# Optimization experiments

Measured on AMD Instinct MI355X. Metric: run time of the kernel, lower is better.

Reference implementation:

```python
import jax, jax.numpy as jnp
import numpy as np

NF = 10      # num RBF / Chebyshev features
GAMMA = 1.0
EMB = 10
H = 64
NHEADS = 2


def _rbf(d):
    centers = jnp.arange(1, NF + 1, dtype=d.dtype)
    return jnp.exp(-GAMMA * (centers - d[..., None]) ** 2)


def _cheb(a):
    feats = [jnp.ones_like(a), a]
    for _ in range(2, NF):
        feats.append(2 * a * feats[-1] - feats[-2])
    return jnp.stack(feats, -1)


def _gru_layer(xs, wih, whh, bih, bhh):
    # xs: [L, B, D] -> [L, B, H]; PyTorch gate order r, z, n
    B = xs.shape[1]
    def step(h, xt):
        gi = xt @ wih.T + bih
        gh = h @ whh.T + bhh
        ir, iz, inn = jnp.split(gi, 3, -1)
        hr, hz, hn = jnp.split(gh, 3, -1)
        r = jax.nn.sigmoid(ir + hr)
        z = jax.nn.sigmoid(iz + hz)
        n = jnp.tanh(inn + r * hn)
        hnew = (1 - z) * n + z * h
        return hnew, hnew
    h0 = jnp.zeros((B, H), xs.dtype)
    _, ys = jax.lax.scan(step, h0, xs)
    return ys


def _mha(x, in_w, in_b, out_w, out_b):
    B, L, E = x.shape
    hd = E // NHEADS
    qkv = x @ in_w.T + in_b
    q, k, v = jnp.split(qkv, 3, -1)
    sp = lambda t: t.reshape(B, L, NHEADS, hd).transpose(0, 2, 1, 3)
    q, k, v = sp(q), sp(k), sp(v)
    scale = 1.0 / float(np.sqrt(hd))
    att = jax.nn.softmax(jnp.einsum('bhqd,bhkd->bhqk', q, k) * scale, -1)
    o = jnp.einsum('bhqk,bhkd->bhqd', att, v).transpose(0, 2, 1, 3).reshape(B, L, E)
    return o @ out_w.T + out_b


def _ln(x, s, b):
    m = x.mean(-1, keepdims=True)
    v = ((x - m) ** 2).mean(-1, keepdims=True)
    return (x - m) / jnp.sqrt(v + 1e-5) * s + b


def setup_inputs() -> dict:
    key = jax.random.key(0)
    ks = jax.random.split(key, 48)
    N, L = 384, 256
    # bond rows: [atom_idx1, atom_idx2, bond_dist]; angle rows: [d1, d2, angle]
    idx1 = jax.random.randint(ks[0], (N, L), 1, 119).astype(jnp.float32)
    idx2 = jax.random.randint(ks[1], (N, L), 1, 119).astype(jnp.float32)
    dist = jax.random.uniform(ks[2], (N, L), minval=0.5, maxval=5.0)
    d1 = jax.random.uniform(ks[3], (N, L), minval=0.5, maxval=5.0)
    d2 = jax.random.uniform(ks[4], (N, L), minval=0.5, maxval=5.0)
    ang = jax.random.uniform(ks[5], (N, L), minval=-1.0, maxval=1.0)
    bond_x = jnp.stack([idx1, idx2, dist], 1)
    angle_x = jnp.stack([d1, d2, ang], 1)
    is_angle = (jnp.arange(N) % 3 == 2)
    x = jnp.where(is_angle[:, None, None], angle_x, bond_x)

    def nrm(k, shp, s=0.1):
        return jax.random.normal(k, shp) * s

    D_IN = 2 * EMB + NF  # 30
    inp = {
        'x': x,
        'emb': nrm(ks[6], (119, EMB), 1.0),
        'wih0': nrm(ks[7], (3 * H, D_IN)),
        'whh0': nrm(ks[8], (3 * H, H)),
        'bih0': nrm(ks[9], (3 * H,)),
        'bhh0': nrm(ks[10], (3 * H,)),
        'wih12': nrm(ks[11], (2, 3 * H, H)),
        'whh12': nrm(ks[12], (2, 3 * H, H)),
        'bih12': nrm(ks[13], (2, 3 * H)),
        'bhh12': nrm(ks[14], (2, 3 * H)),
        'in_w1': nrm(ks[15], (3 * H, H)),
        'in_b1': nrm(ks[16], (3 * H,)),
        'out_w1': nrm(ks[17], (H, H)),
        'out_b1': nrm(ks[18], (H,)),
        'in_w2': nrm(ks[19], (3 * H, H)),
        'in_b2': nrm(ks[20], (3 * H,)),
        'out_w2': nrm(ks[21], (H, H)),
        'out_b2': nrm(ks[22], (H,)),
        'ff_w1': nrm(ks[23], (1024, H)),
        'ff_b1': nrm(ks[24], (1024,)),
        'ff_w2': nrm(ks[25], (H, 1024)),
        'ff_b2': nrm(ks[26], (H,)),
        'ln1_s': jnp.ones((H,)), 'ln1_b': jnp.zeros((H,)),
        'ln2_s': jnp.ones((H,)), 'ln2_b': jnp.zeros((H,)),
        'ln3_s': jnp.ones((H,)), 'ln3_b': jnp.zeros((H,)),
        'ln4_s': jnp.ones((H,)), 'ln4_b': jnp.zeros((H,)),
        'fw1': nrm(ks[27], (256, H)), 'fb1': nrm(ks[28], (256,)),
        'fw2': nrm(ks[29], (64, 256)), 'fb2': nrm(ks[30], (64,)),
        'fw3': nrm(ks[31], (32, 64)), 'fb3': nrm(ks[32], (32,)),
        'fw4': nrm(ks[33], (1, 32)), 'fb4': nrm(ks[34], (1,)),
    }
    return inp


def reference(x, emb, wih0, whh0, bih0, bhh0, wih12, whh12, bih12, bhh12,
              in_w1, in_b1, out_w1, out_b1, in_w2, in_b2, out_w2, out_b2,
              ff_w1, ff_b1, ff_w2, ff_b2,
              ln1_s, ln1_b, ln2_s, ln2_b, ln3_s, ln3_b, ln4_s, ln4_b,
              fw1, fb1, fw2, fb2, fw3, fb3, fw4, fb4):
    # Vectorized featurization (replaces the per-triplet Python loop):
    # rows with i%3 in {0,1} are bond rows, i%3==2 are angle rows.
    i1 = jnp.clip(x[:, 0].astype(jnp.int32), 0, 118)
    i2 = jnp.clip(x[:, 1].astype(jnp.int32), 0, 118)
    bond_feat = jnp.concatenate([emb[i1], emb[i2], _rbf(x[:, 2])], -1)
    angle_feat = jnp.concatenate([_rbf(x[:, 0]), _rbf(x[:, 1]), _cheb(x[:, 2])], -1)
    is_angle = (jnp.arange(x.shape[0]) % 3 == 2)
    feat = jnp.where(is_angle[:, None, None], angle_feat, bond_feat)  # [N, L, 30]

    hs = feat.transpose(1, 0, 2)  # [L, N, 30]
    hs = _gru_layer(hs, wih0, whh0, bih0, bhh0)
    for l in range(2):
        hs = _gru_layer(hs, wih12[l], whh12[l], bih12[l], bhh12[l])
    g = hs.transpose(1, 0, 2)  # [N, L, H]

    def ffn(t):
        return jax.nn.relu(jax.nn.relu(t @ ff_w1.T + ff_b1) @ ff_w2.T + ff_b2)

    a = _mha(g, in_w1, in_b1, out_w1, out_b1)
    h = _ln(g + a, ln1_s, ln1_b)
    h = _ln(h + ffn(h), ln2_s, ln2_b)
    a = _mha(h, in_w2, in_b2, out_w2, out_b2)
    h = _ln(a + a, ln3_s, ln3_b)  # faithful to original: attn_out + attn_out
    h = _ln(h + ffn(h), ln4_s, ln4_b)
    o = h[:, -1, :]
    o = jax.nn.silu(o @ fw1.T + fb1)
    o = jax.nn.silu(o @ fw2.T + fb2)
    o = jax.nn.silu(o @ fw3.T + fb3)
    o = o @ fw4.T + fb4
    return o.squeeze(-1)
```

## Files before the change

kernel.cpp:

```cpp
#include <hip/hip_runtime.h>

static constexpr int NB   = 384;
static constexpr int SEQL = 256;
static constexpr int NROWS = NB * SEQL;

typedef short bf16x8 __attribute__((ext_vector_type(8)));
typedef float f32x4  __attribute__((ext_vector_type(4)));

union B8u {
    bf16x8 v;
    ushort us[8];
    uint4  q;
};

union F4u { float4 v; float f[4]; };

__device__ inline ushort f2bf(float f) {
    uint u = __float_as_uint(f);
    uint r = u + 0x7FFFu + ((u >> 16) & 1u);
    return (ushort)(r >> 16);
}

__device__ inline void split8(float4 a, float4 b, B8u& hi, B8u& lo) {
    float f[8] = {a.x, a.y, a.z, a.w, b.x, b.y, b.z, b.w};
    #pragma unroll
    for (int i = 0; i < 8; ++i) {
        ushort h = f2bf(f[i]);
        hi.us[i] = h;
        float fh = __uint_as_float(((uint)h) << 16);
        lo.us[i] = f2bf(f[i] - fh);
    }
}

__global__ __launch_bounds__(256) void split_kernel(
    const float* __restrict__ src, ushort* __restrict__ hi,
    ushort* __restrict__ lo, int n)
{
    int i = blockIdx.x * 256 + threadIdx.x;
    if (i < n) {
        float f = src[i];
        ushort h = f2bf(f);
        hi[i] = h;
        float fh = __uint_as_float(((uint)h) << 16);
        lo[i] = f2bf(f - fh);
    }
}

__global__ __launch_bounds__(192) void featproj_kernel(
    const float* __restrict__ x, const float* __restrict__ emb,
    const float* __restrict__ wih0, const float* __restrict__ bih0,
    float* __restrict__ X)
{
    __shared__ float F[32][33];
    const int tid = threadIdx.x;
    const int m0  = blockIdx.x * 32;

    if (tid < 96) {
        const int r   = tid & 31;
        const int grp = tid >> 5;
        const int m   = m0 + r;
        const int b   = m % NB;
        const int l   = m / NB;
        const float* xb = x + (size_t)b * (3 * SEQL);
        const float x0 = xb[l], x1 = xb[SEQL + l], x2 = xb[2 * SEQL + l];
        const bool is_angle = (b % 3) == 2;
        float o[10];
        if (is_angle) {
            if (grp < 2) {
                const float a = (grp == 0) ? x0 : x1;
                #pragma unroll
                for (int c = 0; c < 10; ++c) { float d = (float)(c + 1) - a; o[c] = __expf(-d * d); }
            } else {
                float t0 = 1.f, t1 = x2;
                o[0] = 1.f; o[1] = x2;
                #pragma unroll
                for (int c = 2; c < 10; ++c) { float t = 2.f * x2 * t1 - t0; o[c] = t; t0 = t1; t1 = t; }
            }
        } else {
            if (grp < 2) {
                const float xv = (grp == 0) ? x0 : x1;
                int idx = (int)xv; idx = idx < 0 ? 0 : (idx > 118 ? 118 : idx);
                #pragma unroll
                for (int c = 0; c < 10; ++c) o[c] = emb[idx * 10 + c];
            } else {
                #pragma unroll
                for (int c = 0; c < 10; ++c) { float d = (float)(c + 1) - x2; o[c] = __expf(-d * d); }
            }
        }
        #pragma unroll
        for (int c = 0; c < 10; ++c) F[r][grp * 10 + c] = o[c];
    }
    __syncthreads();

    float w[30];
    #pragma unroll
    for (int k = 0; k < 30; ++k) w[k] = wih0[tid * 30 + k];
    const float bj = bih0[tid];
    for (int r = 0; r < 32; ++r) {
        float acc = bj;
        #pragma unroll
        for (int k = 0; k < 30; ++k) acc += F[r][k] * w[k];
        X[(size_t)(m0 + r) * 192 + tid] = acc;
    }
}

__global__ __launch_bounds__(256, 1) void gru_mfma(
    const float* __restrict__ X, const ushort* __restrict__ WhhHi,
    const ushort* __restrict__ WhhLo, const float* __restrict__ bhh,
    float* __restrict__ Y, int out_batch_major)
{
    constexpr int PAD = 88;
    __shared__ __align__(16) ushort Hh[2][16][PAD];
    __shared__ __align__(16) ushort Hl[2][16][PAD];

    const int tid  = threadIdx.x;
    const int wt   = tid >> 6;
    const int lane = tid & 63;
    const int c    = lane & 15;
    const int g    = lane >> 4;
    const int b0   = blockIdx.x * 16;

    B8u awh[3][2], awl[3][2];
    #pragma unroll
    for (int gam = 0; gam < 3; ++gam)
        #pragma unroll
        for (int ks = 0; ks < 2; ++ks) {
            size_t off = (size_t)(64 * gam + 16 * wt + c) * 64 + 32 * ks + 8 * g;
            awh[gam][ks].q = *(const uint4*)(WhhHi + off);
            awl[gam][ks].q = *(const uint4*)(WhhLo + off);
        }
    float bg[3][4];
    #pragma unroll
    for (int gam = 0; gam < 3; ++gam)
        #pragma unroll
        for (int r = 0; r < 4; ++r)
            bg[gam][r] = bhh[64 * gam + 16 * wt + 4 * g + r];

    {
        ushort* zh = &Hh[0][0][0];
        ushort* zl = &Hl[0][0][0];
        for (int i = tid; i < 2 * 16 * PAD; i += 256) { zh[i] = 0; zl[i] = 0; }
    }
    float hold[4] = {0.f, 0.f, 0.f, 0.f};

    F4u gi[3];
    {
        const float* xp = X + ((size_t)(b0 + c)) * 192;
        #pragma unroll
        for (int gam = 0; gam < 3; ++gam)
            gi[gam].v = *(const float4*)(xp + 64 * gam + 16 * wt + 4 * g);
    }
    __syncthreads();

    for (int t = 0; t < SEQL; ++t) {
        const int p = t & 1;

        B8u bh[2], bl[2];
        #pragma unroll
        for (int ks = 0; ks < 2; ++ks) {
            const int sl = (4 * ks + g) ^ (c & 7);
            bh[ks].q = *(const uint4*)&Hh[p][c][sl * 8];
            bl[ks].q = *(const uint4*)&Hl[p][c][sl * 8];
        }

        f32x4 acc[3];
        #pragma unroll
        for (int gam = 0; gam < 3; ++gam)
            acc[gam] = (f32x4){bg[gam][0], bg[gam][1], bg[gam][2], bg[gam][3]};
        #pragma unroll
        for (int gam = 0; gam < 3; ++gam)
            #pragma unroll
            for (int ks = 0; ks < 2; ++ks) {
                acc[gam] = __builtin_amdgcn_mfma_f32_16x16x32_bf16(awh[gam][ks].v, bh[ks].v, acc[gam], 0, 0, 0);
                acc[gam] = __builtin_amdgcn_mfma_f32_16x16x32_bf16(awl[gam][ks].v, bh[ks].v, acc[gam], 0, 0, 0);
                acc[gam] = __builtin_amdgcn_mfma_f32_16x16x32_bf16(awh[gam][ks].v, bl[ks].v, acc[gam], 0, 0, 0);
            }

        F4u ngi[3];
        {
            const int tn = (t + 1 < SEQL) ? t + 1 : t;
            const float* xp = X + ((size_t)tn * NB + b0 + c) * 192;
            #pragma unroll
            for (int gam = 0; gam < 3; ++gam)
                ngi[gam].v = *(const float4*)(xp + 64 * gam + 16 * wt + 4 * g);
        }

        float hn4[4];
        #pragma unroll
        for (int r = 0; r < 4; ++r) {
            const float rr = 1.f / (1.f + __expf(-(gi[0].f[r] + acc[0][r])));
            const float zz = 1.f / (1.f + __expf(-(gi[1].f[r] + acc[1][r])));
            const float nn = tanhf(gi[2].f[r] + rr * acc[2][r]);
            hn4[r] = (1.f - zz) * nn + zz * hold[r];
            hold[r] = hn4[r];
        }

        {
            const size_t row = out_batch_major ? ((size_t)(b0 + c) * SEQL + t)
                                               : ((size_t)t * NB + b0 + c);
            *(float4*)&Y[row * 64 + 16 * wt + 4 * g] =
                make_float4(hn4[0], hn4[1], hn4[2], hn4[3]);
        }

        {
            ushort hh[4], hl[4];
            #pragma unroll
            for (int r = 0; r < 4; ++r) {
                ushort h = f2bf(hn4[r]);
                hh[r] = h;
                hl[r] = f2bf(hn4[r] - __uint_as_float(((uint)h) << 16));
            }
            const int sl = (2 * wt + (g >> 1)) ^ (c & 7);
            const int ad = sl * 8 + (g & 1) * 4;
            *(uint2*)&Hh[p ^ 1][c][ad] = make_uint2((uint)hh[0] | ((uint)hh[1] << 16),
                                                    (uint)hh[2] | ((uint)hh[3] << 16));
            *(uint2*)&Hl[p ^ 1][c][ad] = make_uint2((uint)hl[0] | ((uint)hl[1] << 16),
                                                    (uint)hl[2] | ((uint)hl[3] << 16));
        }
        #pragma unroll
        for (int gam = 0; gam < 3; ++gam) gi[gam].v = ngi[gam].v;
        __syncthreads();
    }
}

template<int NCOLS>
__global__ __launch_bounds__(256, 2) void gemm_mfma(
    const float* __restrict__ A, const ushort* __restrict__ Whi,
    const ushort* __restrict__ Wlo, const float* __restrict__ bias,
    float* __restrict__ C)
{
    const int tid = threadIdx.x;
    const int w   = tid >> 6;
    const int lane = tid & 63;
    const int c = lane & 15;
    const int g = lane >> 4;
    const int m0 = blockIdx.x * 128 + 32 * w;

    B8u ah[2][2], al[2][2];
    #pragma unroll
    for (int rm = 0; rm < 2; ++rm) {
        const float* ap = A + (size_t)(m0 + 16 * rm + c) * 64;
        #pragma unroll
        for (int ks = 0; ks < 2; ++ks) {
            float4 v0 = *(const float4*)(ap + 32 * ks + 8 * g);
            float4 v1 = *(const float4*)(ap + 32 * ks + 8 * g + 4);
            split8(v0, v1, ah[rm][ks], al[rm][ks]);
        }
    }

    f32x4 acc[NCOLS / 16][2];
    #pragma unroll
    for (int nt = 0; nt < NCOLS / 16; ++nt) {
        float bv = bias[16 * nt + c];
        #pragma unroll
        for (int rm = 0; rm < 2; ++rm)
            acc[nt][rm] = (f32x4){bv, bv, bv, bv};
    }

    #pragma unroll
    for (int nt = 0; nt < NCOLS / 16; ++nt) {
        B8u wh[2], wl[2];
        #pragma unroll
        for (int ks = 0; ks < 2; ++ks) {
            size_t off = (size_t)(16 * nt + c) * 64 + 32 * ks + 8 * g;
            wh[ks].q = *(const uint4*)(Whi + off);
            wl[ks].q = *(const uint4*)(Wlo + off);
        }
        #pragma unroll
        for (int rm = 0; rm < 2; ++rm)
            #pragma unroll
            for (int ks = 0; ks < 2; ++ks) {
                acc[nt][rm] = __builtin_amdgcn_mfma_f32_16x16x32_bf16(ah[rm][ks].v, wh[ks].v, acc[nt][rm], 0, 0, 0);
                acc[nt][rm] = __builtin_amdgcn_mfma_f32_16x16x32_bf16(al[rm][ks].v, wh[ks].v, acc[nt][rm], 0, 0, 0);
                acc[nt][rm] = __builtin_amdgcn_mfma_f32_16x16x32_bf16(ah[rm][ks].v, wl[ks].v, acc[nt][rm], 0, 0, 0);
            }
    }

    #pragma unroll
    for (int nt = 0; nt < NCOLS / 16; ++nt)
        #pragma unroll
        for (int rm = 0; rm < 2; ++rm)
            #pragma unroll
            for (int reg = 0; reg < 4; ++reg) {
                int row = m0 + 16 * rm + 4 * g + reg;
                C[(size_t)row * NCOLS + 16 * nt + c] = acc[nt][rm][reg];
            }
}

__global__ __launch_bounds__(256, 2) void ffn_mfma(
    const float* __restrict__ Xin,
    const ushort* __restrict__ W1hi, const ushort* __restrict__ W1lo,
    const ushort* __restrict__ W2hi, const ushort* __restrict__ W2lo,
    const float* __restrict__ b1, const float* __restrict__ b2,
    float* __restrict__ Out)
{
    __shared__ __align__(16) ushort sW1h[64 * 72], sW1l[64 * 72];
    __shared__ __align__(16) ushort sW2h[64 * 72], sW2l[64 * 72];
    __shared__ __align__(16) ushort sHh[128 * 72], sHl[128 * 72];
    __shared__ float sb1[64];

    const int tid = threadIdx.x;
    const int w   = tid >> 6;
    const int lane = tid & 63;
    const int c = lane & 15;
    const int g = lane >> 4;
    const int r0 = blockIdx.x * 128;

    B8u xh[2][2], xl[2][2];
    #pragma unroll
    for (int rm = 0; rm < 2; ++rm) {
        const float* ap = Xin + (size_t)(r0 + 32 * w + 16 * rm + c) * 64;
        #pragma unroll
        for (int ks = 0; ks < 2; ++ks) {
            float4 v0 = *(const float4*)(ap + 32 * ks + 8 * g);
            float4 v1 = *(const float4*)(ap + 32 * ks + 8 * g + 4);
            split8(v0, v1, xh[rm][ks], xl[rm][ks]);
        }
    }

    f32x4 acc2[4][2];
    #pragma unroll
    for (int jt = 0; jt < 4; ++jt) {
        float bv = b2[16 * jt + c];
        #pragma unroll
        for (int mt = 0; mt < 2; ++mt)
            acc2[jt][mt] = (f32x4){bv, bv, bv, bv};
    }

    for (int nc = 0; nc < 16; ++nc) {
        __syncthreads();
        {
            const int n = tid >> 2, s = tid & 3;
            size_t s1 = (size_t)(nc * 64 + n) * 64 + s * 16;
            size_t s2 = (size_t)n * 1024 + nc * 64 + s * 16;
            int d = n * 72 + s * 16;
            *(uint4*)&sW1h[d]     = *(const uint4*)(W1hi + s1);
            *(uint4*)&sW1h[d + 8] = *(const uint4*)(W1hi + s1 + 8);
            *(uint4*)&sW1l[d]     = *(const uint4*)(W1lo + s1);
            *(uint4*)&sW1l[d + 8] = *(const uint4*)(W1lo + s1 + 8);
            *(uint4*)&sW2h[d]     = *(const uint4*)(W2hi + s2);
            *(uint4*)&sW2h[d + 8] = *(const uint4*)(W2hi + s2 + 8);
            *(uint4*)&sW2l[d]     = *(const uint4*)(W2lo + s2);
            *(uint4*)&sW2l[d + 8] = *(const uint4*)(W2lo + s2 + 8);
            if (tid < 64) sb1[tid] = b1[nc * 64 + tid];
        }
        __syncthreads();

        f32x4 acc1[4][2];
        #pragma unroll
        for (int jm = 0; jm < 4; ++jm) {
            float b0 = sb1[16 * jm + 4 * g + 0];
            float b1v = sb1[16 * jm + 4 * g + 1];
            float b2v = sb1[16 * jm + 4 * g + 2];
            float b3v = sb1[16 * jm + 4 * g + 3];
            #pragma unroll
            for (int rm = 0; rm < 2; ++rm)
                acc1[jm][rm] = (f32x4){b0, b1v, b2v, b3v};
        }
        #pragma unroll
        for (int jm = 0; jm < 4; ++jm) {
            B8u w1h[2], w1l[2];
            #pragma unroll
            for (int ks = 0; ks < 2; ++ks) {
                int off = (16 * jm + c) * 72 + 32 * ks + 8 * g;
                w1h[ks].q = *(const uint4*)&sW1h[off];
                w1l[ks].q = *(const uint4*)&sW1l[off];
            }
            #pragma unroll
            for (int rm = 0; rm < 2; ++rm)
                #pragma unroll
                for (int ks = 0; ks < 2; ++ks) {
                    acc1[jm][rm] = __builtin_amdgcn_mfma_f32_16x16x32_bf16(w1h[ks].v, xh[rm][ks].v, acc1[jm][rm], 0, 0, 0);
                    acc1[jm][rm] = __builtin_amdgcn_mfma_f32_16x16x32_bf16(w1l[ks].v, xh[rm][ks].v, acc1[jm][rm], 0, 0, 0);
                    acc1[jm][rm] = __builtin_amdgcn_mfma_f32_16x16x32_bf16(w1h[ks].v, xl[rm][ks].v, acc1[jm][rm], 0, 0, 0);
                }
        }
        #pragma unroll
        for (int jm = 0; jm < 4; ++jm)
            #pragma unroll
            for (int rm = 0; rm < 2; ++rm) {
                ushort hh[4], hl[4];
                #pragma unroll
                for (int reg = 0; reg < 4; ++reg) {
                    float hv = fmaxf(acc1[jm][rm][reg], 0.f);
                    ushort h = f2bf(hv);
                    hh[reg] = h;
                    float fh = __uint_as_float(((uint)h) << 16);
                    hl[reg] = f2bf(hv - fh);
                }
                int el = (32 * w + 16 * rm + c) * 72 + 16 * jm + 4 * g;
                *(uint2*)&sHh[el] = make_uint2((uint)hh[0] | ((uint)hh[1] << 16),
                                               (uint)hh[2] | ((uint)hh[3] << 16));
                *(uint2*)&sHl[el] = make_uint2((uint)hl[0] | ((uint)hl[1] << 16),
                                               (uint)hl[2] | ((uint)hl[3] << 16));
            }
        asm volatile("s_waitcnt lgkmcnt(0)" ::: "memory");
        __builtin_amdgcn_sched_barrier(0);

        #pragma unroll
        for (int ks = 0; ks < 2; ++ks) {
            B8u ahh[2], ahl[2], bwh[4], bwl[4];
            #pragma unroll
            for (int mt = 0; mt < 2; ++mt) {
                int el = (32 * w + 16 * mt + c) * 72 + 32 * ks + 8 * g;
                ahh[mt].q = *(const uint4*)&sHh[el];
                ahl[mt].q = *(const uint4*)&sHl[el];
            }
            #pragma unroll
            for (int jt = 0; jt < 4; ++jt) {
                int el = (16 * jt + c) * 72 + 32 * ks + 8 * g;
                bwh[jt].q = *(const uint4*)&sW2h[el];
                bwl[jt].q = *(const uint4*)&sW2l[el];
            }
            #pragma unroll
            for (int jt = 0; jt < 4; ++jt)
                #pragma unroll
                for (int mt = 0; mt < 2; ++mt) {
                    acc2[jt][mt] = __builtin_amdgcn_mfma_f32_16x16x32_bf16(ahh[mt].v, bwh[jt].v, acc2[jt][mt], 0, 0, 0);
                    acc2[jt][mt] = __builtin_amdgcn_mfma_f32_16x16x32_bf16(ahl[mt].v, bwh[jt].v, acc2[jt][mt], 0, 0, 0);
                    acc2[jt][mt] = __builtin_amdgcn_mfma_f32_16x16x32_bf16(ahh[mt].v, bwl[jt].v, acc2[jt][mt], 0, 0, 0);
                }
        }
    }

    #pragma unroll
    for (int jt = 0; jt < 4; ++jt)
        #pragma unroll
        for (int mt = 0; mt < 2; ++mt)
            #pragma unroll
            for (int reg = 0; reg < 4; ++reg) {
                int row = r0 + 32 * w + 16 * mt + 4 * g + reg;
                Out[(size_t)row * 64 + 16 * jt + c] = fmaxf(acc2[jt][mt][reg], 0.f);
            }
}

__global__ __launch_bounds__(256, 2) void attn_mfma(
    const float* __restrict__ QKV, float* __restrict__ Out)
{
    __shared__ __align__(16) ushort Ph[4][4096];
    __shared__ __align__(16) ushort Pl[4][4096];

    const int h = blockIdx.x;
    const int b = blockIdx.y;
    const int tid = threadIdx.x;
    const int w = tid >> 6;
    const int lane = tid & 63;
    const int c = lane & 15;
    const int g = lane >> 4;
    const float scale = 0.17677669529663687f;

    const float* base = QKV + (size_t)b * SEQL * 192;
    ushort* phw = Ph[w];
    ushort* plw = Pl[w];

    B8u qh[4], ql[4];
    #pragma unroll
    for (int qt = 0; qt < 4; ++qt) {
        const float* p = base + (size_t)(64 * w + 16 * qt + c) * 192 + h * 32 + 8 * g;
        float4 v0 = *(const float4*)p;
        float4 v1 = *(const float4*)(p + 4);
        v0.x *= scale; v0.y *= scale; v0.z *= scale; v0.w *= scale;
        v1.x *= scale; v1.y *= scale; v1.z *= scale; v1.w *= scale;
        split8(v0, v1, qh[qt], ql[qt]);
    }

    f32x4 o[2][4];
    #pragma unroll
    for (int dt = 0; dt < 2; ++dt)
        #pragma unroll
        for (int qt = 0; qt < 4; ++qt)
            o[dt][qt] = (f32x4){0.f, 0.f, 0.f, 0.f};
    float mrun[4] = {-1e30f, -1e30f, -1e30f, -1e30f};
    float lrun[4] = {0.f, 0.f, 0.f, 0.f};

    for (int kc = 0; kc < 4; ++kc) {
        B8u kh[4], kl[4];
        #pragma unroll
        for (int kt = 0; kt < 4; ++kt) {
            const float* p = base + (size_t)(kc * 64 + 16 * kt + c) * 192 + 64 + h * 32 + 8 * g;
            split8(*(const float4*)p, *(const float4*)(p + 4), kh[kt], kl[kt]);
        }
        f32x4 st[4][4];
        #pragma unroll
        for (int kt = 0; kt < 4; ++kt)
            #pragma unroll
            for (int qt = 0; qt < 4; ++qt)
                st[kt][qt] = (f32x4){0.f, 0.f, 0.f, 0.f};
        #pragma unroll
        for (int kt = 0; kt < 4; ++kt)
            #pragma unroll
            for (int qt = 0; qt < 4; ++qt) {
                st[kt][qt] = __builtin_amdgcn_mfma_f32_16x16x32_bf16(kh[kt].v, qh[qt].v, st[kt][qt], 0, 0, 0);
                st[kt][qt] = __builtin_amdgcn_mfma_f32_16x16x32_bf16(kl[kt].v, qh[qt].v, st[kt][qt], 0, 0, 0);
                st[kt][qt] = __builtin_amdgcn_mfma_f32_16x16x32_bf16(kh[kt].v, ql[qt].v, st[kt][qt], 0, 0, 0);
            }

        asm volatile("s_waitcnt lgkmcnt(0)" ::: "memory");
        #pragma unroll
        for (int qt = 0; qt < 4; ++qt) {
            float cmax = st[0][qt][0];
            #pragma unroll
            for (int kt = 0; kt < 4; ++kt)
                #pragma unroll
                for (int r = 0; r < 4; ++r) cmax = fmaxf(cmax, st[kt][qt][r]);
            cmax = fmaxf(cmax, __shfl_xor(cmax, 16));
            cmax = fmaxf(cmax, __shfl_xor(cmax, 32));
            const float mnew = fmaxf(mrun[qt], cmax);
            const float corr = __expf(mrun[qt] - mnew);
            mrun[qt] = mnew;
            const int ql_ = 16 * qt + c;
            float csum = 0.f;
            #pragma unroll
            for (int kt = 0; kt < 4; ++kt) {
                ushort hh[4], hl[4];
                #pragma unroll
                for (int r = 0; r < 4; ++r) {
                    float pv = __expf(st[kt][qt][r] - mnew);
                    csum += pv;
                    ushort ph_ = f2bf(pv);
                    hh[r] = ph_;
                    hl[r] = f2bf(pv - __uint_as_float(((uint)ph_) << 16));
                }
                const int ow = (2 * kt + (g >> 1)) ^ (ql_ & 7);
                const int addr = ql_ * 64 + ow * 8 + (g & 1) * 4;
                *(uint2*)&phw[addr] = make_uint2((uint)hh[0] | ((uint)hh[1] << 16),
                                                 (uint)hh[2] | ((uint)hh[3] << 16));
                *(uint2*)&plw[addr] = make_uint2((uint)hl[0] | ((uint)hl[1] << 16),
                                                 (uint)hl[2] | ((uint)hl[3] << 16));
            }
            csum += __shfl_xor(csum, 16);
            csum += __shfl_xor(csum, 32);
            lrun[qt] = lrun[qt] * corr + csum;
            #pragma unroll
            for (int dt = 0; dt < 2; ++dt)
                #pragma unroll
                for (int r = 0; r < 4; ++r) o[dt][qt][r] *= corr;
        }

        B8u vh[2][2], vl[2][2];
        #pragma unroll
        for (int ks = 0; ks < 2; ++ks)
            #pragma unroll
            for (int dt = 0; dt < 2; ++dt) {
                const float* vp = base + (size_t)(kc * 64 + ks * 32 + 8 * g) * 192 + 128 + h * 32 + 16 * dt + c;
                float f0 = vp[0], f1 = vp[192], f2 = vp[384], f3 = vp[576];
                float f4 = vp[768], f5 = vp[960], f6 = vp[1152], f7 = vp[1344];
                split8(make_float4(f0, f1, f2, f3), make_float4(f4, f5, f6, f7),
                       vh[ks][dt], vl[ks][dt]);
            }

        asm volatile("s_waitcnt lgkmcnt(0)" ::: "memory");
        __builtin_amdgcn_sched_barrier(0);

        #pragma unroll
        for (int ks = 0; ks < 2; ++ks)
            #pragma unroll
            for (int qt = 0; qt < 4; ++qt) {
                const int ql_ = 16 * qt + c;
                const int orr = (ks * 4 + g) ^ (ql_ & 7);
                const int addr = ql_ * 64 + orr * 8;
                B8u pbh, pbl;
                pbh.q = *(const uint4*)&phw[addr];
                pbl.q = *(const uint4*)&plw[addr];
                #pragma unroll
                for (int dt = 0; dt < 2; ++dt) {
                    o[dt][qt] = __builtin_amdgcn_mfma_f32_16x16x32_bf16(vh[ks][dt].v, pbh.v, o[dt][qt], 0, 0, 0);
                    o[dt][qt] = __builtin_amdgcn_mfma_f32_16x16x32_bf16(vl[ks][dt].v, pbh.v, o[dt][qt], 0, 0, 0);
                    o[dt][qt] = __builtin_amdgcn_mfma_f32_16x16x32_bf16(vh[ks][dt].v, pbl.v, o[dt][qt], 0, 0, 0);
                }
            }
    }

    #pragma unroll
    for (int qt = 0; qt < 4; ++qt) {
        const float inv = 1.f / lrun[qt];
        const size_t row = (size_t)b * SEQL + 64 * w + 16 * qt + c;
        #pragma unroll
        for (int dt = 0; dt < 2; ++dt)
            #pragma unroll
            for (int r = 0; r < 4; ++r)
                Out[row * 64 + h * 32 + 16 * dt + 4 * g + r] = o[dt][qt][r] * inv;
    }
}

__global__ __launch_bounds__(256) void add_ln_kernel(
    const float* __restrict__ A, const float* __restrict__ B,
    const float* __restrict__ s, const float* __restrict__ bb,
    float* __restrict__ O)
{
    const size_t row = (size_t)blockIdx.x * 4 + (threadIdx.x >> 6);
    const int lane = threadIdx.x & 63;
    float v = A[row * 64 + lane] + B[row * 64 + lane];
    float sum = v;
    #pragma unroll
    for (int off = 32; off; off >>= 1) sum += __shfl_xor(sum, off);
    const float mean = sum * (1.f / 64.f);
    const float d = v - mean;
    float sq = d * d;
    #pragma unroll
    for (int off = 32; off; off >>= 1) sq += __shfl_xor(sq, off);
    const float var = sq * (1.f / 64.f);
    O[row * 64 + lane] = d * rsqrtf(var + 1e-5f) * s[lane] + bb[lane];
}

__global__ __launch_bounds__(256) void head_kernel(
    const float* __restrict__ Hf,
    const float* __restrict__ fw1, const float* __restrict__ fb1,
    const float* __restrict__ fw2, const float* __restrict__ fb2,
    const float* __restrict__ fw3, const float* __restrict__ fb3,
    const float* __restrict__ fw4, const float* __restrict__ fb4,
    float* __restrict__ out)
{
    const int b = blockIdx.x;
    const int tid = threadIdx.x;
    __shared__ float t0[64], t1[256], t2[64], t3[32];
    if (tid < 64) t0[tid] = Hf[((size_t)b * SEQL + (SEQL - 1)) * 64 + tid];
    __syncthreads();
    {
        float acc = fb1[tid];
        #pragma unroll 4
        for (int k = 0; k < 64; ++k) acc += t0[k] * fw1[tid * 64 + k];
        t1[tid] = acc / (1.f + __expf(-acc));
    }
    __syncthreads();
    if (tid < 64) {
        float acc = fb2[tid];
        #pragma unroll 4
        for (int k = 0; k < 256; ++k) acc += t1[k] * fw2[tid * 256 + k];
        t2[tid] = acc / (1.f + __expf(-acc));
    }
    __syncthreads();
    if (tid < 32) {
        float acc = fb3[tid];
        #pragma unroll 4
        for (int k = 0; k < 64; ++k) acc += t2[k] * fw3[tid * 64 + k];
        t3[tid] = acc / (1.f + __expf(-acc));
    }
    __syncthreads();
    if (tid == 0) {
        float acc = fb4[0];
        #pragma unroll
        for (int k = 0; k < 32; ++k) acc += t3[k] * fw4[k];
        out[b] = acc;
    }
}

extern "C" void kernel_launch(void* const* d_in, const int* in_sizes, int n_in,
                              void* d_out, int out_size, void* d_ws, size_t ws_size,
                              hipStream_t stream) {
    const float* x     = (const float*)d_in[0];
    const float* emb   = (const float*)d_in[1];
    const float* wih0  = (const float*)d_in[2];
    const float* whh0  = (const float*)d_in[3];
    const float* bih0  = (const float*)d_in[4];
    const float* bhh0  = (const float*)d_in[5];
    const float* wih12 = (const float*)d_in[6];
    const float* whh12 = (const float*)d_in[7];
    const float* bih12 = (const float*)d_in[8];
    const float* bhh12 = (const float*)d_in[9];
    const float* in_w1 = (const float*)d_in[10];
    const float* in_b1 = (const float*)d_in[11];
    const float* out_w1= (const float*)d_in[12];
    const float* out_b1= (const float*)d_in[13];
    const float* in_w2 = (const float*)d_in[14];
    const float* in_b2 = (const float*)d_in[15];
    const float* out_w2= (const float*)d_in[16];
    const float* out_b2= (const float*)d_in[17];
    const float* ff_w1 = (const float*)d_in[18];
    const float* ff_b1 = (const float*)d_in[19];
    const float* ff_w2 = (const float*)d_in[20];
    const float* ff_b2 = (const float*)d_in[21];
    const float* ln1_s = (const float*)d_in[22];
    const float* ln1_b = (const float*)d_in[23];
    const float* ln2_s = (const float*)d_in[24];
    const float* ln2_b = (const float*)d_in[25];
    const float* ln3_s = (const float*)d_in[26];
    const float* ln3_b = (const float*)d_in[27];
    const float* ln4_s = (const float*)d_in[28];
    const float* ln4_b = (const float*)d_in[29];
    const float* fw1   = (const float*)d_in[30];
    const float* fb1   = (const float*)d_in[31];
    const float* fw2   = (const float*)d_in[32];
    const float* fb2   = (const float*)d_in[33];
    const float* fw3   = (const float*)d_in[34];
    const float* fb3   = (const float*)d_in[35];
    const float* fw4   = (const float*)d_in[36];
    const float* fb4   = (const float*)d_in[37];

    float* ws = (float*)d_ws;
    float* X  = ws;
    float* S0 = X  + (size_t)NROWS * 192;
    float* S1 = S0 + (size_t)NROWS * 64;
    float* S2 = S1 + (size_t)NROWS * 64;

    ushort* bf = (ushort*)(S2 + (size_t)NROWS * 64);
    ushort* ffw1hi = bf;
    ushort* ffw1lo = ffw1hi + 65536;
    ushort* ffw2hi = ffw1lo + 65536;
    ushort* ffw2lo = ffw2hi + 65536;
    ushort* wghi   = ffw2lo + 65536;
    ushort* wglo   = wghi + 24576;
    ushort* q1hi   = wglo + 24576;
    ushort* q1lo   = q1hi + 12288;
    ushort* q2hi   = q1lo + 12288;
    ushort* q2lo   = q2hi + 12288;
    ushort* o1hi   = q2lo + 12288;
    ushort* o1lo   = o1hi + 4096;
    ushort* o2hi   = o1lo + 4096;
    ushort* o2lo   = o2hi + 4096;
    ushort* w0hi   = o2lo + 4096;
    ushort* w0lo   = w0hi + 12288;
    ushort* w12hi  = w0lo + 12288;
    ushort* w12lo  = w12hi + 24576;

    split_kernel<<<65536 / 256, 256, 0, stream>>>(ff_w1, ffw1hi, ffw1lo, 65536);
    split_kernel<<<65536 / 256, 256, 0, stream>>>(ff_w2, ffw2hi, ffw2lo, 65536);
    split_kernel<<<24576 / 256, 256, 0, stream>>>(wih12, wghi, wglo, 24576);
    split_kernel<<<12288 / 256, 256, 0, stream>>>(in_w1, q1hi, q1lo, 12288);
    split_kernel<<<12288 / 256, 256, 0, stream>>>(in_w2, q2hi, q2lo, 12288);
    split_kernel<<<4096 / 256, 256, 0, stream>>>(out_w1, o1hi, o1lo, 4096);
    split_kernel<<<4096 / 256, 256, 0, stream>>>(out_w2, o2hi, o2lo, 4096);
    split_kernel<<<12288 / 256, 256, 0, stream>>>(whh0, w0hi, w0lo, 12288);
    split_kernel<<<24576 / 256, 256, 0, stream>>>(whh12, w12hi, w12lo, 24576);

    featproj_kernel<<<NROWS / 32, 192, 0, stream>>>(x, emb, wih0, bih0, X);
    gru_mfma<<<NB / 16, 256, 0, stream>>>(X, w0hi, w0lo, bhh0, S0, 0);
    gemm_mfma<192><<<NROWS / 128, 256, 0, stream>>>(S0, wghi, wglo, bih12, X);
    gru_mfma<<<NB / 16, 256, 0, stream>>>(X, w12hi, w12lo, bhh12, S1, 0);
    gemm_mfma<192><<<NROWS / 128, 256, 0, stream>>>(S1, wghi + 12288, wglo + 12288, bih12 + 192, X);
    gru_mfma<<<NB / 16, 256, 0, stream>>>(X, w12hi + 12288, w12lo + 12288, bhh12 + 192, S0, 1);

    gemm_mfma<192><<<NROWS / 128, 256, 0, stream>>>(S0, q1hi, q1lo, in_b1, X);
    attn_mfma<<<dim3(2, NB), 256, 0, stream>>>(X, S1);
    gemm_mfma<64><<<NROWS / 128, 256, 0, stream>>>(S1, o1hi, o1lo, out_b1, S2);
    add_ln_kernel<<<NROWS / 4, 256, 0, stream>>>(S0, S2, ln1_s, ln1_b, S1);
    ffn_mfma<<<NROWS / 128, 256, 0, stream>>>(S1, ffw1hi, ffw1lo, ffw2hi, ffw2lo, ff_b1, ff_b2, S2);
    add_ln_kernel<<<NROWS / 4, 256, 0, stream>>>(S1, S2, ln2_s, ln2_b, S0);

    gemm_mfma<192><<<NROWS / 128, 256, 0, stream>>>(S0, q2hi, q2lo, in_b2, X);
    attn_mfma<<<dim3(2, NB), 256, 0, stream>>>(X, S1);
    gemm_mfma<64><<<NROWS / 128, 256, 0, stream>>>(S1, o2hi, o2lo, out_b2, S2);
    add_ln_kernel<<<NROWS / 4, 256, 0, stream>>>(S2, S2, ln3_s, ln3_b, S1);
    ffn_mfma<<<NROWS / 128, 256, 0, stream>>>(S1, ffw1hi, ffw1lo, ffw2hi, ffw2lo, ff_b1, ff_b2, S2);
    add_ln_kernel<<<NROWS / 4, 256, 0, stream>>>(S1, S2, ln4_s, ln4_b, S0);

    head_kernel<<<NB, 256, 0, stream>>>(S0, fw1, fb1, fw2, fb2, fw3, fb3, fw4, fb4,
                                        (float*)d_out);
    (void)in_sizes; (void)n_in; (void)out_size; (void)ws_size;
}
```

Baseline: 1.253 ms.

## Shorten GRU recurrence critical path with split accumulators and fast activations

```diff
diff --git a/kernel.cpp b/kernel.cpp
--- a/kernel.cpp
+++ b/kernel.cpp
@@ -30,6 +30,20 @@
         float fh = __uint_as_float(((uint)h) << 16);
         lo.us[i] = f2bf(f[i] - fh);
     }
+}
+
+__device__ inline float fast_rcp(float x) {
+    float r = __builtin_amdgcn_rcpf(x);
+    return r * (2.f - x * r);
+}
+__device__ inline float fast_sig(float x) {
+    float e = __expf(fminf(-x, 80.f));
+    return fast_rcp(1.f + e);
+}
+__device__ inline float fast_tanh(float a) {
+    float e = __expf(fminf(2.f * fabsf(a), 80.f));
+    float t = 1.f - 2.f * fast_rcp(1.f + e);
+    return (a >= 0.f) ? t : -t;
 }
 
 __global__ __launch_bounds__(256) void split_kernel(
@@ -163,18 +177,21 @@
             bl[ks].q = *(const uint4*)&Hl[p][c][sl * 8];
         }
 
-        f32x4 acc[3];
-        #pragma unroll
-        for (int gam = 0; gam < 3; ++gam)
-            acc[gam] = (f32x4){bg[gam][0], bg[gam][1], bg[gam][2], bg[gam][3]};
-        #pragma unroll
-        for (int gam = 0; gam < 3; ++gam)
-            #pragma unroll
-            for (int ks = 0; ks < 2; ++ks) {
-                acc[gam] = __builtin_amdgcn_mfma_f32_16x16x32_bf16(awh[gam][ks].v, bh[ks].v, acc[gam], 0, 0, 0);
-                acc[gam] = __builtin_amdgcn_mfma_f32_16x16x32_bf16(awl[gam][ks].v, bh[ks].v, acc[gam], 0, 0, 0);
-                acc[gam] = __builtin_amdgcn_mfma_f32_16x16x32_bf16(awh[gam][ks].v, bl[ks].v, acc[gam], 0, 0, 0);
-            }
+        f32x4 a0[3], a1[3];
+        #pragma unroll
+        for (int gam = 0; gam < 3; ++gam) {
+            a0[gam] = (f32x4){bg[gam][0], bg[gam][1], bg[gam][2], bg[gam][3]};
+            a1[gam] = (f32x4){0.f, 0.f, 0.f, 0.f};
+        }
+        #pragma unroll
+        for (int gam = 0; gam < 3; ++gam) {
+            a0[gam] = __builtin_amdgcn_mfma_f32_16x16x32_bf16(awh[gam][0].v, bh[0].v, a0[gam], 0, 0, 0);
+            a1[gam] = __builtin_amdgcn_mfma_f32_16x16x32_bf16(awh[gam][1].v, bh[1].v, a1[gam], 0, 0, 0);
+            a0[gam] = __builtin_amdgcn_mfma_f32_16x16x32_bf16(awl[gam][0].v, bh[0].v, a0[gam], 0, 0, 0);
+            a1[gam] = __builtin_amdgcn_mfma_f32_16x16x32_bf16(awl[gam][1].v, bh[1].v, a1[gam], 0, 0, 0);
+            a0[gam] = __builtin_amdgcn_mfma_f32_16x16x32_bf16(awh[gam][0].v, bl[0].v, a0[gam], 0, 0, 0);
+            a1[gam] = __builtin_amdgcn_mfma_f32_16x16x32_bf16(awh[gam][1].v, bl[1].v, a1[gam], 0, 0, 0);
+        }
 
         F4u ngi[3];
         {
@@ -188,9 +205,12 @@
         float hn4[4];
         #pragma unroll
         for (int r = 0; r < 4; ++r) {
-            const float rr = 1.f / (1.f + __expf(-(gi[0].f[r] + acc[0][r])));
-            const float zz = 1.f / (1.f + __expf(-(gi[1].f[r] + acc[1][r])));
-            const float nn = tanhf(gi[2].f[r] + rr * acc[2][r]);
+            const float gr = a0[0][r] + a1[0][r];
+            const float gz = a0[1][r] + a1[1][r];
+            const float gn = a0[2][r] + a1[2][r];
+            const float rr = fast_sig(gi[0].f[r] + gr);
+            const float zz = fast_sig(gi[1].f[r] + gz);
+            const float nn = fast_tanh(gi[2].f[r] + rr * gn);
             hn4[r] = (1.f - zz) * nn + zz * hold[r];
             hold[r] = hn4[r];
         }
@@ -219,7 +239,11 @@
         }
         #pragma unroll
         for (int gam = 0; gam < 3; ++gam) gi[gam].v = ngi[gam].v;
-        __syncthreads();
+
+        asm volatile("s_waitcnt lgkmcnt(0)" ::: "memory");
+        __builtin_amdgcn_sched_barrier(0);
+        __builtin_amdgcn_s_barrier();
+        __builtin_amdgcn_sched_barrier(0);
     }
 }
 
```

Measured after the change: 1.120 ms. 10.6% less time.
